# Kernel tuning notes

Measured on AMD Instinct MI355X. Metric: run time of the kernel, lower is better.

The kernel has to match this reference:

```python
import jax, jax.numpy as jnp
import numpy as np

B, IN, H = 65536, 256, 512

def setup_inputs() -> dict:
    key = jax.random.key(0)
    ks = jax.random.split(key, 10)
    inp = {
        "x": jax.random.normal(ks[0], (B, IN), dtype=jnp.float32),
        "h_prev": jax.random.normal(ks[1], (B, H), dtype=jnp.float32),
        "c_prev": jax.random.normal(ks[2], (B, H), dtype=jnp.float32),
        "n_prev": jax.random.uniform(ks[3], (B, H), dtype=jnp.float32),
        "m_prev": jax.random.normal(ks[4], (B, H), dtype=jnp.float32),
        "w_f": jax.random.normal(ks[5], (IN, H), dtype=jnp.float32) * 0.05,
        "w_c": jax.random.normal(ks[6], (IN, H), dtype=jnp.float32) * 0.05,
        "r_f": jax.random.normal(ks[7], (H, H), dtype=jnp.float32) * 0.05,
        "r_c": jax.random.normal(ks[8], (H, H), dtype=jnp.float32) * 0.05,
        "b_f": jnp.zeros((H,), dtype=jnp.float32),
        "b_c": jnp.zeros((H,), dtype=jnp.float32),
    }
    return inp

def reference(x, h_prev, c_prev, n_prev, m_prev, w_f, w_c, r_f, r_c, b_f, b_c):
    # f_t = exp(pre_f); log(f_t) = pre_f, so stabilizer works on pre-activations.
    pre_f = x @ w_f + h_prev @ r_f + b_f          # [B, H]
    c_tilda = x @ w_c + h_prev @ r_c + b_c        # [B, H]
    # m_t = max(log f_t + m_prev, log(exp(0))) = max(pre_f + m_prev, 0)
    m_t = jnp.maximum(pre_f + m_prev, 0.0)
    i_prime = jnp.exp(-m_t)
    f_prime = jnp.exp(pre_f + m_prev - m_t)
    c_t = f_prime * c_prev + i_prime * jnp.tanh(c_tilda)
    n_t = f_prime * n_prev + i_prime
    h_t = jnp.tanh(c_t / jnp.maximum(n_t, 1e-8))
    return (h_t, c_t, n_t, m_t)
```

## Files before the change

### kernel.cpp

```cpp
#include <hip/hip_runtime.h>

#define B_SZ   65536
#define IN_SZ  256
#define H_SZ   512
#define K_SZ   768
#define BM     128
#define BN     128
#define BK     64
#define LDK    72

typedef __attribute__((ext_vector_type(4))) float  f32x4;
typedef __attribute__((ext_vector_type(8))) __bf16 bf16x8;

__device__ __forceinline__ unsigned short f2bf(float f) {
    unsigned u = __float_as_uint(f);
    u += 0x7FFFu + ((u >> 16) & 1u);
    return (unsigned short)(u >> 16);
}

__device__ __forceinline__ float tanh_fast(float x) {
    x = fminf(fmaxf(x, -16.0f), 16.0f);
    float e = __expf(2.0f * x);
    return (e - 1.0f) / (e + 1.0f);
}

__global__ void prep_weights(const float* __restrict__ w_f, const float* __restrict__ w_c,
                             const float* __restrict__ r_f, const float* __restrict__ r_c,
                             unsigned short* __restrict__ wt) {
    int id = blockIdx.x * 256 + threadIdx.x;
    int n  = id / K_SZ;
    int k  = id - n * K_SZ;
    int col = n & (H_SZ - 1);
    float v;
    if (n < H_SZ) v = (k < IN_SZ) ? w_f[k * H_SZ + col] : r_f[(k - IN_SZ) * H_SZ + col];
    else          v = (k < IN_SZ) ? w_c[k * H_SZ + col] : r_c[(k - IN_SZ) * H_SZ + col];
    wt[(size_t)n * K_SZ + k] = f2bf(v);
}

__launch_bounds__(256, 2)
__global__ void smgu_kernel(const float* __restrict__ x, const float* __restrict__ h_prev,
                            const float* __restrict__ c_prev, const float* __restrict__ n_prev,
                            const float* __restrict__ m_prev,
                            const float* __restrict__ b_f, const float* __restrict__ b_c,
                            const unsigned short* __restrict__ wt,
                            float* __restrict__ out) {
    __shared__ unsigned short sA[BM * LDK];
    __shared__ unsigned short sF[BN * LDK];
    __shared__ unsigned short sC[BN * LDK];

    const int tid    = threadIdx.x;
    const int bid    = (blockIdx.x & 7) * 256 + (blockIdx.x >> 3);
    const int tile_m = bid >> 2;
    const int tile_n = bid & 3;
    const int m0 = tile_m * BM;
    const int n0 = tile_n * BN;

    const int lane = tid & 63;
    const int wave = tid >> 6;
    const int wm = (wave >> 1) * 64;
    const int wn = (wave & 1) * 64;

    const int fr = lane & 15;
    const int fg = (lane >> 4) * 8;

    f32x4 accF[4][4];
    f32x4 accC[4][4];
#pragma unroll
    for (int i = 0; i < 4; ++i)
#pragma unroll
        for (int j = 0; j < 4; ++j) { accF[i][j] = (f32x4)0.0f; accC[i][j] = (f32x4)0.0f; }

    for (int kb = 0; kb < K_SZ; kb += BK) {
        {
            const float* src; int ldsrc, kloc;
            if (kb < IN_SZ) { src = x;      ldsrc = IN_SZ; kloc = kb; }
            else            { src = h_prev; ldsrc = H_SZ;  kloc = kb - IN_SZ; }
#pragma unroll
            for (int j = 0; j < 8; ++j) {
                int idx = tid + 256 * j;
                int row = idx >> 4, c4 = idx & 15;
                const float4 v = *(const float4*)&src[(size_t)(m0 + row) * ldsrc + kloc + c4 * 4];
                ushort4 b;
                b.x = f2bf(v.x); b.y = f2bf(v.y); b.z = f2bf(v.z); b.w = f2bf(v.w);
                *(ushort4*)&sA[row * LDK + c4 * 4] = b;
            }
        }
#pragma unroll
        for (int j = 0; j < 4; ++j) {
            int idx = tid + 256 * j;
            int row = idx >> 3, c8 = idx & 7;
            uint4 vf = *(const uint4*)&wt[(size_t)(n0 + row) * K_SZ + kb + c8 * 8];
            *(uint4*)&sF[row * LDK + c8 * 8] = vf;
            uint4 vc = *(const uint4*)&wt[(size_t)(H_SZ + n0 + row) * K_SZ + kb + c8 * 8];
            *(uint4*)&sC[row * LDK + c8 * 8] = vc;
        }
        __syncthreads();

#pragma unroll
        for (int ks = 0; ks < BK; ks += 32) {
            bf16x8 af[4], bf[4], bc[4];
#pragma unroll
            for (int mi = 0; mi < 4; ++mi)
                af[mi] = *(const bf16x8*)&sA[(wm + mi * 16 + fr) * LDK + ks + fg];
#pragma unroll
            for (int ni = 0; ni < 4; ++ni) {
                bf[ni] = *(const bf16x8*)&sF[(wn + ni * 16 + fr) * LDK + ks + fg];
                bc[ni] = *(const bf16x8*)&sC[(wn + ni * 16 + fr) * LDK + ks + fg];
            }
#pragma unroll
            for (int mi = 0; mi < 4; ++mi)
#pragma unroll
                for (int ni = 0; ni < 4; ++ni) {
                    accF[mi][ni] = __builtin_amdgcn_mfma_f32_16x16x32_bf16(af[mi], bf[ni], accF[mi][ni], 0, 0, 0);
                    accC[mi][ni] = __builtin_amdgcn_mfma_f32_16x16x32_bf16(af[mi], bc[ni], accC[mi][ni], 0, 0, 0);
                }
        }
        __syncthreads();
    }

    const size_t BH = (size_t)B_SZ * H_SZ;
#pragma unroll
    for (int ni = 0; ni < 4; ++ni) {
        int col = n0 + wn + ni * 16 + fr;
        float bfv = b_f[col], bcv = b_c[col];
#pragma unroll
        for (int mi = 0; mi < 4; ++mi) {
            int row0 = m0 + wm + mi * 16 + (lane >> 4) * 4;
#pragma unroll
            for (int r = 0; r < 4; ++r) {
                size_t idx = (size_t)(row0 + r) * H_SZ + col;
                float pre_f = accF[mi][ni][r] + bfv;
                float pre_c = accC[mi][ni][r] + bcv;
                float mp = m_prev[idx];
                float s  = pre_f + mp;
                float m_t = fmaxf(s, 0.0f);
                float ip  = __expf(-m_t);
                float fp  = __expf(s - m_t);
                float cp  = c_prev[idx];
                float np  = n_prev[idx];
                float c_t = fp * cp + ip * tanh_fast(pre_c);
                float n_t = fp * np + ip;
                float h_t = tanh_fast(c_t / fmaxf(n_t, 1e-8f));
                out[idx]          = h_t;
                out[BH + idx]     = c_t;
                out[2 * BH + idx] = n_t;
                out[3 * BH + idx] = m_t;
            }
        }
    }
}

extern "C" void kernel_launch(void* const* d_in, const int* in_sizes, int n_in,
                              void* d_out, int out_size, void* d_ws, size_t ws_size,
                              hipStream_t stream) {
    const float* x      = (const float*)d_in[0];
    const float* h_prev = (const float*)d_in[1];
    const float* c_prev = (const float*)d_in[2];
    const float* n_prev = (const float*)d_in[3];
    const float* m_prev = (const float*)d_in[4];
    const float* w_f    = (const float*)d_in[5];
    const float* w_c    = (const float*)d_in[6];
    const float* r_f    = (const float*)d_in[7];
    const float* r_c    = (const float*)d_in[8];
    const float* b_f    = (const float*)d_in[9];
    const float* b_c    = (const float*)d_in[10];
    float* out = (float*)d_out;
    unsigned short* wt = (unsigned short*)d_ws;

    prep_weights<<<(2 * H_SZ * K_SZ) / 256, 256, 0, stream>>>(w_f, w_c, r_f, r_c, wt);
    smgu_kernel<<<(B_SZ / BM) * (H_SZ / BN), 256, 0, stream>>>(
        x, h_prev, c_prev, n_prev, m_prev, b_f, b_c, wt, out);
}
```

Baseline: 1.312 ms.

## Prefetch next K-chunk tiles into registers while computing the current chunk

```diff
diff --git a/kernel.cpp b/kernel.cpp
--- a/kernel.cpp
+++ b/kernel.cpp
@@ -8,6 +8,7 @@
 #define BN     128
 #define BK     64
 #define LDK    72
+#define NCHUNK (K_SZ / BK)
 
 typedef __attribute__((ext_vector_type(4))) float  f32x4;
 typedef __attribute__((ext_vector_type(8))) __bf16 bf16x8;
@@ -70,31 +71,48 @@
 #pragma unroll
         for (int j = 0; j < 4; ++j) { accF[i][j] = (f32x4)0.0f; accC[i][j] = (f32x4)0.0f; }
 
-    for (int kb = 0; kb < K_SZ; kb += BK) {
-        {
-            const float* src; int ldsrc, kloc;
-            if (kb < IN_SZ) { src = x;      ldsrc = IN_SZ; kloc = kb; }
-            else            { src = h_prev; ldsrc = H_SZ;  kloc = kb - IN_SZ; }
+    const int r0a = tid >> 4;
+    const int c4a = tid & 15;
+    const int r0w = tid >> 3;
+    const int c8w = tid & 7;
+
+    f32x4 pA[8];
+    uint4 pF[4], pC[4];
+
+    auto load_tiles = [&](int kb) {
+        const float* src; int ldsrc, kloc;
+        if (kb < IN_SZ) { src = x;      ldsrc = IN_SZ; kloc = kb; }
+        else            { src = h_prev; ldsrc = H_SZ;  kloc = kb - IN_SZ; }
 #pragma unroll
-            for (int j = 0; j < 8; ++j) {
-                int idx = tid + 256 * j;
-                int row = idx >> 4, c4 = idx & 15;
-                const float4 v = *(const float4*)&src[(size_t)(m0 + row) * ldsrc + kloc + c4 * 4];
-                ushort4 b;
-                b.x = f2bf(v.x); b.y = f2bf(v.y); b.z = f2bf(v.z); b.w = f2bf(v.w);
-                *(ushort4*)&sA[row * LDK + c4 * 4] = b;
-            }
+        for (int j = 0; j < 8; ++j)
+            pA[j] = *(const f32x4*)&src[(size_t)(m0 + r0a + 16 * j) * ldsrc + kloc + c4a * 4];
+#pragma unroll
+        for (int j = 0; j < 4; ++j) {
+            pF[j] = *(const uint4*)&wt[(size_t)(n0 + r0w + 32 * j) * K_SZ + kb + c8w * 8];
+            pC[j] = *(const uint4*)&wt[(size_t)(H_SZ + n0 + r0w + 32 * j) * K_SZ + kb + c8w * 8];
+        }
+    };
+    auto store_tiles = [&]() {
+#pragma unroll
+        for (int j = 0; j < 8; ++j) {
+            ushort4 b;
+            b.x = f2bf(pA[j][0]); b.y = f2bf(pA[j][1]);
+            b.z = f2bf(pA[j][2]); b.w = f2bf(pA[j][3]);
+            *(ushort4*)&sA[(r0a + 16 * j) * LDK + c4a * 4] = b;
         }
 #pragma unroll
         for (int j = 0; j < 4; ++j) {
-            int idx = tid + 256 * j;
-            int row = idx >> 3, c8 = idx & 7;
-            uint4 vf = *(const uint4*)&wt[(size_t)(n0 + row) * K_SZ + kb + c8 * 8];
-            *(uint4*)&sF[row * LDK + c8 * 8] = vf;
-            uint4 vc = *(const uint4*)&wt[(size_t)(H_SZ + n0 + row) * K_SZ + kb + c8 * 8];
-            *(uint4*)&sC[row * LDK + c8 * 8] = vc;
+            *(uint4*)&sF[(r0w + 32 * j) * LDK + c8w * 8] = pF[j];
+            *(uint4*)&sC[(r0w + 32 * j) * LDK + c8w * 8] = pC[j];
         }
+    };
+
+    load_tiles(0);
+
+    for (int t = 0; t < NCHUNK; ++t) {
+        store_tiles();
         __syncthreads();
+        if (t + 1 < NCHUNK) load_tiles((t + 1) * BK);
 
 #pragma unroll
         for (int ks = 0; ks < BK; ks += 32) {
@@ -120,12 +138,12 @@
 
     const size_t BH = (size_t)B_SZ * H_SZ;
 #pragma unroll
-    for (int ni = 0; ni < 4; ++ni) {
-        int col = n0 + wn + ni * 16 + fr;
-        float bfv = b_f[col], bcv = b_c[col];
+    for (int mi = 0; mi < 4; ++mi) {
+        int row0 = m0 + wm + mi * 16 + (lane >> 4) * 4;
 #pragma unroll
-        for (int mi = 0; mi < 4; ++mi) {
-            int row0 = m0 + wm + mi * 16 + (lane >> 4) * 4;
+        for (int ni = 0; ni < 4; ++ni) {
+            int col = n0 + wn + ni * 16 + fr;
+            float bfv = b_f[col], bcv = b_c[col];
 #pragma unroll
             for (int r = 0; r < 4; ++r) {
                 size_t idx = (size_t)(row0 + r) * H_SZ + col;
```

After: 1.172 ms. 1.12x faster.
